# Kernel optimization log

Hardware: AMD Instinct MI355X
Metric: run time of the kernel (lower is better)

## Reference

```python
import jax, jax.numpy as jnp
import numpy as np

C = 1024      # channels
K = 7         # kernel_size
G = 1         # groups (G>1 crashes in the original torch code; see notes)
GC = C // G   # group_channels
OFFSET_SCALE = 2.0
LN_EPS = 1e-5


def setup_inputs() -> dict:
    key = jax.random.key(0)
    ks = jax.random.split(key, 8)
    N, L = 4, 2048
    s = 1.0 / np.sqrt(C)
    x = jax.random.normal(ks[0], (N, L, C), jnp.float32)
    Wi = jax.random.normal(ks[1], (C, C), jnp.float32) * s
    bi = jnp.zeros((C,), jnp.float32)
    dw_w = jax.random.normal(ks[2], (C, 1, 3), jnp.float32) * 0.5   # depthwise conv kernel (O, I/g=1, W)
    dw_b = jnp.zeros((C,), jnp.float32)
    ln_g = jnp.ones((C,), jnp.float32)
    ln_b = jnp.zeros((C,), jnp.float32)
    Wo = jax.random.normal(ks[3], (G * K, C), jnp.float32) * 0.02   # offset head (nonzero to exercise gather)
    bo = jnp.zeros((G * K,), jnp.float32)
    Wm = jax.random.normal(ks[4], (G * K, C), jnp.float32) * 0.02   # mask head
    bm = jnp.zeros((G * K,), jnp.float32)
    Wout = jax.random.normal(ks[5], (C, C), jnp.float32) * s
    bout = jnp.zeros((C,), jnp.float32)
    return {"x": x, "Wi": Wi, "bi": bi, "dw_w": dw_w, "dw_b": dw_b,
            "ln_g": ln_g, "ln_b": ln_b, "Wo": Wo, "bo": bo,
            "Wm": Wm, "bm": bm, "Wout": Wout, "bout": bout}


def _forward(x, Wi, bi, dw_w, dw_b, ln_g, ln_b, Wo, bo, Wm, bm, Wout, bout):
    N, L, Cc = x.shape
    dt = x.dtype
    # input projection
    x_proj = x @ Wi.T + bi                                  # [N,L,C]
    # depthwise conv (k=3, pad=1, groups=C) -> LayerNorm(C) -> GELU(exact)
    y = jax.lax.conv_general_dilated(
        x.transpose(0, 2, 1), dw_w, window_strides=(1,), padding=((1, 1),),
        dimension_numbers=("NCH", "OIH", "NCH"), feature_group_count=Cc)
    x_dw = y.transpose(0, 2, 1) + dw_b                       # [N,L,C]
    mu = x_dw.mean(-1, keepdims=True)
    var = ((x_dw - mu) ** 2).mean(-1, keepdims=True)
    x_dw = (x_dw - mu) * jax.lax.rsqrt(var + LN_EPS) * ln_g + ln_b
    x_dw = jax.nn.gelu(x_dw, approximate=False)
    # dynamic offsets and sampling mask
    offsets = (x_dw @ Wo.T + bo).reshape(N, L, G, K) * OFFSET_SCALE
    mask = jax.nn.softmax((x_dw @ Wm.T + bm).reshape(N, L, G, K), axis=-1)
    mask = jnp.nan_to_num(mask, nan=0.0)
    # absolute sampling positions
    ref_off = jnp.linspace(-(K // 2), K // 2, K).astype(dt)          # [K]
    pos = jnp.arange(L, dtype=dt)[None, :, None, None]               # [1,L,1,1]
    abs_pos = pos + ref_off[None, None, None, :] + offsets           # [N,L,G,K]
    apc = jnp.clip(abs_pos, 0.0, L - 1)
    p_floor = jnp.clip(apc.astype(jnp.int32), 0, L - 1)
    p_ceil = jnp.clip(p_floor + 1, 0, L - 1)
    w_ceil = apc - p_floor.astype(dt)
    w_floor = 1.0 - w_ceil
    valid = jnp.logical_not((abs_pos < 0) | (abs_pos > L - 1)).astype(dt)
    w_floor = w_floor * valid
    w_ceil = w_ceil * valid
    # gather + bilinear blend (G=1: each sample index grabs the full C channels)
    idx_f = p_floor.reshape(N, -1)[:, :, None]                       # [N, L*G*K, 1]
    idx_c = p_ceil.reshape(N, -1)[:, :, None]
    v_floor = jnp.take_along_axis(x_proj, idx_f, axis=1).reshape(N, L, G, K, GC)
    v_ceil = jnp.take_along_axis(x_proj, idx_c, axis=1).reshape(N, L, G, K, GC)
    sampled = v_floor * w_floor[..., None] + v_ceil * w_ceil[..., None]
    out = (sampled * mask[..., None]).sum(axis=3).reshape(N, L, Cc)  # sum over K
    return out @ Wout.T + bout


def reference(x, Wi, bi, dw_w, dw_b, ln_g, ln_b, Wo, bo, Wm, bm, Wout, bout):
    return _forward(x, Wi, bi, dw_w, dw_b, ln_g, ln_b, Wo, bo, Wm, bm, Wout, bout)
```

## Files before the change

### kernel.cpp

```cpp
#include <hip/hip_runtime.h>
#include <hip/hip_bf16.h>
#include <cstdint>

#define C_DIM 1024
#define L_DIM 2048
#define N_DIM 4
#define M_DIM (N_DIM * L_DIM)

typedef __attribute__((ext_vector_type(8))) short frag8;
typedef __attribute__((ext_vector_type(4)))  float f32x4;
typedef __attribute__((ext_vector_type(16))) float f32x16;

__device__ __forceinline__ void gl_lds16(const void* g, void* l) {
  __builtin_amdgcn_global_load_lds((const __attribute__((address_space(1))) void*)g,
                                   (__attribute__((address_space(3))) void*)l,
                                   16, 0, 0);
}
__device__ __forceinline__ void store_out(float* Y, size_t idx, float v) { Y[idx] = v; }
__device__ __forceinline__ void store_out(__hip_bfloat16* Y, size_t idx, float v) {
  Y[idx] = __float2bfloat16(v);
}
__device__ __forceinline__ float4 ldbf4(const __hip_bfloat16* p) {
  union { short4 s; __hip_bfloat16 h[4]; } u; u.s = *(const short4*)p;
  return make_float4((float)u.h[0], (float)u.h[1], (float)u.h[2], (float)u.h[3]);
}
__device__ __forceinline__ void stbf4(__hip_bfloat16* p, float4 v) {
  union { short4 s; __hip_bfloat16 h[4]; } u;
  u.h[0] = __float2bfloat16(v.x); u.h[1] = __float2bfloat16(v.y);
  u.h[2] = __float2bfloat16(v.z); u.h[3] = __float2bfloat16(v.w);
  *(short4*)p = u.s;
}
__device__ __forceinline__ float gelu_fast(float t) {
  const float t3 = t * t * t;
  const float ns = -1.5957691216f * t - 0.0713548163f * t3;
  return t / (1.f + __expf(ns));
}

__global__ __launch_bounds__(256)
void cvt_f32_bf16(const float* __restrict__ in, __hip_bfloat16* __restrict__ out, int n8) {
  const int i = blockIdx.x * 256 + threadIdx.x;
  if (i >= n8) return;
  const float4 a = *(const float4*)(in + (size_t)i * 8);
  const float4 b = *(const float4*)(in + (size_t)i * 8 + 4);
  union { __hip_bfloat16 h[8]; int4 q; } u;
  u.h[0] = __float2bfloat16(a.x); u.h[1] = __float2bfloat16(a.y);
  u.h[2] = __float2bfloat16(a.z); u.h[3] = __float2bfloat16(a.w);
  u.h[4] = __float2bfloat16(b.x); u.h[5] = __float2bfloat16(b.y);
  u.h[6] = __float2bfloat16(b.z); u.h[7] = __float2bfloat16(b.w);
  *(int4*)(out + (size_t)i * 8) = u.q;
}

__global__ __launch_bounds__(256)
void cvt_two_f32_bf16(const float* __restrict__ inA, __hip_bfloat16* __restrict__ outA,
                      const float* __restrict__ inB, __hip_bfloat16* __restrict__ outB,
                      int n8each) {
  int i = blockIdx.x * 256 + threadIdx.x;
  const float* in; __hip_bfloat16* out;
  if (i < n8each) { in = inA; out = outA; }
  else            { in = inB; out = outB; i -= n8each; }
  if (i >= n8each) return;
  const float4 a = *(const float4*)(in + (size_t)i * 8);
  const float4 b = *(const float4*)(in + (size_t)i * 8 + 4);
  union { __hip_bfloat16 h[8]; int4 q; } u;
  u.h[0] = __float2bfloat16(a.x); u.h[1] = __float2bfloat16(a.y);
  u.h[2] = __float2bfloat16(a.z); u.h[3] = __float2bfloat16(a.w);
  u.h[4] = __float2bfloat16(b.x); u.h[5] = __float2bfloat16(b.y);
  u.h[6] = __float2bfloat16(b.z); u.h[7] = __float2bfloat16(b.w);
  *(int4*)(out + (size_t)i * 8) = u.q;
}

__global__ __launch_bounds__(256)
void cvt_trans_wi(const float* __restrict__ Wi, __hip_bfloat16* __restrict__ WiT) {
  __shared__ float tile[64][65];
  const int bi = blockIdx.x;
  const int bj = blockIdx.y;
  const int t  = threadIdx.x;
  const int r  = t >> 2;
  const int c0 = (t & 3) * 16;
  const float* src = Wi + (size_t)(bi * 64 + r) * C_DIM + bj * 64 + c0;
  *(float4*)&tile[r][c0]      = *(const float4*)(src);
  *(float4*)&tile[r][c0 + 4]  = *(const float4*)(src + 4);
  *(float4*)&tile[r][c0 + 8]  = *(const float4*)(src + 8);
  *(float4*)&tile[r][c0 + 12] = *(const float4*)(src + 12);
  __syncthreads();
  const int kr = t >> 2, j0 = (t & 3) * 16;
  __hip_bfloat16* dst = WiT + (size_t)(bj * 64 + kr) * C_DIM + bi * 64 + j0;
  union { __hip_bfloat16 h[16]; int4 q[2]; } u;
#pragma unroll
  for (int i = 0; i < 16; i++) u.h[i] = __float2bfloat16(tile[j0 + i][kr]);
  *(int4*)(dst)     = u.q[0];
  *(int4*)(dst + 8) = u.q[1];
}

__global__ __launch_bounds__(256)
void cvt_wout_bvec(const float* __restrict__ Wout, __hip_bfloat16* __restrict__ Woutb,
                   const float* __restrict__ bi, float* __restrict__ bvec) {
  const int b = blockIdx.x;
  if (b < 512) {
    const int i = b * 256 + threadIdx.x;
    const float4 a = *(const float4*)(Wout + (size_t)i * 8);
    const float4 c = *(const float4*)(Wout + (size_t)i * 8 + 4);
    union { __hip_bfloat16 h[8]; int4 q; } u;
    u.h[0] = __float2bfloat16(a.x); u.h[1] = __float2bfloat16(a.y);
    u.h[2] = __float2bfloat16(a.z); u.h[3] = __float2bfloat16(a.w);
    u.h[4] = __float2bfloat16(c.x); u.h[5] = __float2bfloat16(c.y);
    u.h[6] = __float2bfloat16(c.z); u.h[7] = __float2bfloat16(c.w);
    *(int4*)(Woutb + (size_t)i * 8) = u.q;
  } else {
    const int row  = (b - 512) * 4 + (threadIdx.x >> 6);
    const int lane = threadIdx.x & 63;
    const float* wr = Wout + (size_t)row * C_DIM;
    float s = 0.f;
#pragma unroll
    for (int c = 0; c < 4; c++) {
      const int j = c * 256 + lane * 4;
      const float4 w  = *(const float4*)(wr + j);
      const float4 bb = *(const float4*)(bi + j);
      s += w.x * bb.x + w.y * bb.y + w.z * bb.z + w.w * bb.w;
    }
#pragma unroll
    for (int m = 1; m < 64; m <<= 1) s += __shfl_xor(s, m);
    if (lane == 0) bvec[row] = s;
  }
}

template <typename TY>
__global__ __launch_bounds__(256, 2)
void gemm_db(const __hip_bfloat16* __restrict__ X,
             const __hip_bfloat16* __restrict__ W,
             const float* __restrict__ bias,
             TY* __restrict__ Y, int M, int N, int K,
             const float* __restrict__ sArr, const float* __restrict__ bvec)
{
  __shared__ __hip_bfloat16 As[2][2][128 * 32];
  __shared__ __hip_bfloat16 Bs[2][2][128 * 32];
  const int tid  = threadIdx.x;
  const int lane = tid & 63;
  const int wave = tid >> 6;
  const int bm = blockIdx.x * 128;
  const int bn = blockIdx.y * 128;
  const int wr = (wave >> 1) * 64;
  const int wc = (wave & 1) * 64;
  const int srow  = tid >> 2;
  const int skoff = (tid & 3) * 8;

  const __hip_bfloat16* gA0 = X + (size_t)(bm + srow) * K + skoff;
  const __hip_bfloat16* gA1 = X + (size_t)(bm + 64 + srow) * K + skoff;
  const __hip_bfloat16* gB0 = W + (size_t)(bn + srow) * K + skoff;
  const __hip_bfloat16* gB1 = W + (size_t)(bn + 64 + srow) * K + skoff;

  f32x16 acc[2][2] = {};
  const int arow  = lane & 31;
  const int akoff = (lane >> 5) * 8;

#define STAGE(k0, buf)                                        \
  do {                                                        \
    gl_lds16(gA0 + (k0),      &As[buf][0][tid * 8]);          \
    gl_lds16(gA1 + (k0),      &As[buf][0][2048 + tid * 8]);   \
    gl_lds16(gA0 + (k0) + 32, &As[buf][1][tid * 8]);          \
    gl_lds16(gA1 + (k0) + 32, &As[buf][1][2048 + tid * 8]);   \
    gl_lds16(gB0 + (k0),      &Bs[buf][0][tid * 8]);          \
    gl_lds16(gB1 + (k0),      &Bs[buf][0][2048 + tid * 8]);   \
    gl_lds16(gB0 + (k0) + 32, &Bs[buf][1][tid * 8]);          \
    gl_lds16(gB1 + (k0) + 32, &Bs[buf][1][2048 + tid * 8]);   \
  } while (0)

  STAGE(0, 0);
  __syncthreads();
  const int iters = K / 64;
  for (int it = 0; it < iters; ++it) {
    const int cur = it & 1;
    if (it + 1 < iters) STAGE((it + 1) * 64, cur ^ 1);

#pragma unroll
    for (int p = 0; p < 2; ++p)
#pragma unroll
      for (int h = 0; h < 2; ++h) {
        const frag8 a0 = *(const frag8*)&As[cur][p][(wr + arow) * 32 + h * 16 + akoff];
        const frag8 a1 = *(const frag8*)&As[cur][p][(wr + 32 + arow) * 32 + h * 16 + akoff];
        const frag8 b0 = *(const frag8*)&Bs[cur][p][(wc + arow) * 32 + h * 16 + akoff];
        const frag8 b1 = *(const frag8*)&Bs[cur][p][(wc + 32 + arow) * 32 + h * 16 + akoff];
        acc[0][0] = __builtin_amdgcn_mfma_f32_32x32x16_bf16(a0, b0, acc[0][0], 0, 0, 0);
        acc[0][1] = __builtin_amdgcn_mfma_f32_32x32x16_bf16(a0, b1, acc[0][1], 0, 0, 0);
        acc[1][0] = __builtin_amdgcn_mfma_f32_32x32x16_bf16(a1, b0, acc[1][0], 0, 0, 0);
        acc[1][1] = __builtin_amdgcn_mfma_f32_32x32x16_bf16(a1, b1, acc[1][1], 0, 0, 0);
      }
    __syncthreads();
  }
#undef STAGE

#pragma unroll
  for (int i = 0; i < 2; i++)
#pragma unroll
    for (int j = 0; j < 2; j++) {
      const int col = bn + wc + j * 32 + (lane & 31);
      const float bv  = bias ? bias[col] : 0.f;
      const float bvv = (sArr && bvec) ? bvec[col] : 0.f;
#pragma unroll
      for (int r = 0; r < 16; r++) {
        const int row = bm + wr + i * 32 + (r & 3) + 8 * (r >> 2) + 4 * (lane >> 5);
        float extra = bv;
        if (sArr) extra += sArr[row] * bvv;
        store_out(Y, (size_t)row * N + col, acc[i][j][r] + extra);
      }
    }
}

struct Ld8f { float4 a, b; };
struct Ld8b { int4 a; };
__device__ __forceinline__ Ld8f ld8(const float* p) {
  return { *(const float4*)p, *(const float4*)(p + 4) };
}
__device__ __forceinline__ Ld8b ld8(const __hip_bfloat16* p) { return { *(const int4*)p }; }
__device__ __forceinline__ void st8(__hip_bfloat16* l, const Ld8f& v) {
  union { __hip_bfloat16 h[8]; int4 q; } u;
  u.h[0] = __float2bfloat16(v.a.x); u.h[1] = __float2bfloat16(v.a.y);
  u.h[2] = __float2bfloat16(v.a.z); u.h[3] = __float2bfloat16(v.a.w);
  u.h[4] = __float2bfloat16(v.b.x); u.h[5] = __float2bfloat16(v.b.y);
  u.h[6] = __float2bfloat16(v.b.z); u.h[7] = __float2bfloat16(v.b.w);
  *(int4*)l = u.q;
}
__device__ __forceinline__ void st8(__hip_bfloat16* l, const Ld8b& v) { *(int4*)l = v.a; }

template <typename TX, typename TY>
__global__ __launch_bounds__(256, 2)
void gemm_nt(const TX* __restrict__ X, const float* __restrict__ W,
             const float* __restrict__ bias, TY* __restrict__ Y, int M, int N, int K)
{
  __shared__ __hip_bfloat16 As[128 * 32];
  __shared__ __hip_bfloat16 Bs[128 * 32];
  const int tid  = threadIdx.x;
  const int lane = tid & 63;
  const int wave = tid >> 6;
  const int bm = blockIdx.x * 128;
  const int bn = blockIdx.y * 128;
  const int wr = (wave >> 1) * 64;
  const int wc = (wave & 1) * 64;
  const int srow  = tid >> 2;
  const int skoff = (tid & 3) * 8;

  f32x4 acc[4][4] = {};
  const TX*    gA0 = X + (size_t)(bm + srow) * K + skoff;
  const TX*    gA1 = X + (size_t)(bm + 64 + srow) * K + skoff;
  const float* gB0 = W + (size_t)(bn + srow) * K + skoff;
  const float* gB1 = W + (size_t)(bn + 64 + srow) * K + skoff;
  const int arow  = lane & 15;
  const int akoff = (lane >> 4) * 8;

  for (int k0 = 0; k0 < K; k0 += 32) {
    const auto va0 = ld8(gA0 + k0);
    const auto va1 = ld8(gA1 + k0);
    const auto vb0 = ld8(gB0 + k0);
    const auto vb1 = ld8(gB1 + k0);
    __syncthreads();
    st8(&As[srow * 32 + skoff],        va0);
    st8(&As[(64 + srow) * 32 + skoff], va1);
    st8(&Bs[srow * 32 + skoff],        vb0);
    st8(&Bs[(64 + srow) * 32 + skoff], vb1);
    __syncthreads();

    frag8 a[4], b[4];
#pragma unroll
    for (int i = 0; i < 4; i++)
      a[i] = *(const frag8*)&As[(wr + i * 16 + arow) * 32 + akoff];
#pragma unroll
    for (int j = 0; j < 4; j++)
      b[j] = *(const frag8*)&Bs[(wc + j * 16 + arow) * 32 + akoff];
#pragma unroll
    for (int i = 0; i < 4; i++)
#pragma unroll
      for (int j = 0; j < 4; j++)
        acc[i][j] = __builtin_amdgcn_mfma_f32_16x16x32_bf16(a[i], b[j], acc[i][j], 0, 0, 0);
  }
#pragma unroll
  for (int i = 0; i < 4; i++)
#pragma unroll
    for (int j = 0; j < 4; j++) {
      const int col = bn + wc + j * 16 + (lane & 15);
      const float bv = bias[col];
#pragma unroll
      for (int r = 0; r < 4; r++) {
        const int row = bm + wr + i * 16 + (lane >> 4) * 4 + r;
        store_out(Y, (size_t)row * N + col, acc[i][j][r] + bv);
      }
    }
}

__global__ __launch_bounds__(512, 2)
void pre_fused_v4(const float* __restrict__ x,
                  const float* __restrict__ dw_w, const float* __restrict__ dw_b,
                  const float* __restrict__ ln_g, const float* __restrict__ ln_b,
                  const float* __restrict__ Wo,   const float* __restrict__ bo,
                  const float* __restrict__ Wm,   const float* __restrict__ bmb,
                  __hip_bfloat16* __restrict__ xbb,
                  float* __restrict__ coef)
{
  __shared__ float sW[16384];
  float* sWo  = sW;
  float* sWm  = sW + 7168;
  float* slng = sW + 14336;
  float* slnb = sW + 15360;

  const int tid  = threadIdx.x;
  const int lane = tid & 63;
  const int wid  = tid >> 6;

#pragma unroll
  for (int i = 0; i < 3; i++) {
    gl_lds16(Wo + (size_t)(i * 512 + tid) * 4, &sWo[(i * 512 + tid) * 4]);
    gl_lds16(Wm + (size_t)(i * 512 + tid) * 4, &sWm[(i * 512 + tid) * 4]);
  }
  if (tid < 256) {
    gl_lds16(Wo + (size_t)(1536 + tid) * 4, &sWo[(1536 + tid) * 4]);
    gl_lds16(Wm + (size_t)(1536 + tid) * 4, &sWm[(1536 + tid) * 4]);
    gl_lds16(ln_g + (size_t)tid * 4, &slng[tid * 4]);
  } else {
    const int t = tid - 256;
    gl_lds16(ln_b + (size_t)t * 4, &slnb[t * 4]);
  }
  __syncthreads();

  const int b    = blockIdx.x;
  const int bs   = (b & 7) * 64 + (b >> 3);
  const int row0 = bs * 16 + wid * 2;
  const int l0   = row0 & (L_DIM - 1);

  const float* xr = x + (size_t)row0 * C_DIM;

  float4 v[2][4];
#pragma unroll
  for (int j = 0; j < 4; j++) {
    const int c4 = j * 256 + lane * 4;
    float4 xv[4];
#pragma unroll
    for (int m = 0; m < 4; m++) {
      const int lm = l0 + m - 1;
      if (lm >= 0 && lm < L_DIM)
        xv[m] = *(const float4*)(xr + ((long)m - 1) * C_DIM + c4);
      else
        xv[m] = make_float4(0.f, 0.f, 0.f, 0.f);
    }
#pragma unroll
    for (int r = 0; r < 2; r++)
      stbf4(xbb + (size_t)(row0 + r) * C_DIM + c4, xv[r + 1]);

    const float4 w0 = *(const float4*)(dw_w + (size_t)c4 * 3);
    const float4 w1 = *(const float4*)(dw_w + (size_t)c4 * 3 + 4);
    const float4 w2 = *(const float4*)(dw_w + (size_t)c4 * 3 + 8);
    const float4 bb = *(const float4*)(dw_b + c4);
#pragma unroll
    for (int r = 0; r < 2; r++) {
      const float4 xm = xv[r], x0 = xv[r + 1], xq = xv[r + 2];
      v[r][j].x = xm.x * w0.x + x0.x * w0.y + xq.x * w0.z + bb.x;
      v[r][j].y = xm.y * w0.w + x0.y * w1.x + xq.y * w1.y + bb.y;
      v[r][j].z = xm.z * w1.z + x0.z * w1.w + xq.z * w2.x + bb.z;
      v[r][j].w = xm.w * w2.y + x0.w * w2.z + xq.w * w2.w + bb.w;
    }
  }

  float mu[2], rstd[2];
#pragma unroll
  for (int r = 0; r < 2; r++) {
    float s1 = 0.f, s2 = 0.f;
#pragma unroll
    for (int j = 0; j < 4; j++) {
      s1 += v[r][j].x + v[r][j].y + v[r][j].z + v[r][j].w;
      s2 += v[r][j].x * v[r][j].x + v[r][j].y * v[r][j].y
          + v[r][j].z * v[r][j].z + v[r][j].w * v[r][j].w;
    }
    const float t1 = s1 + __shfl_xor(s1, 32);
    const float t2 = s2 + __shfl_xor(s2, 32);
    float cc = (lane < 32) ? t1 : t2;
#pragma unroll
    for (int m = 16; m >= 1; m >>= 1) cc += __shfl_xor(cc, m);
    const float dd = __shfl_xor(cc, 32);
    const float S1 = (lane < 32) ? cc : dd;
    const float S2 = (lane < 32) ? dd : cc;
    mu[r]   = S1 * (1.f / C_DIM);
    rstd[r] = rsqrtf(S2 * (1.f / C_DIM) - mu[r] * mu[r] + 1e-5f);
  }

  float po[2][7] = {}, pm[2][7] = {};
#pragma unroll
  for (int j = 0; j < 4; j++) {
    const int c4 = j * 256 + lane * 4;
    const float4 gg = *(const float4*)&slng[c4];
    const float4 bb = *(const float4*)&slnb[c4];
    float4 g[2];
#pragma unroll
    for (int r = 0; r < 2; r++) {
      g[r].x = gelu_fast((v[r][j].x - mu[r]) * rstd[r] * gg.x + bb.x);
      g[r].y = gelu_fast((v[r][j].y - mu[r]) * rstd[r] * gg.y + bb.y);
      g[r].z = gelu_fast((v[r][j].z - mu[r]) * rstd[r] * gg.z + bb.z);
      g[r].w = gelu_fast((v[r][j].w - mu[r]) * rstd[r] * gg.w + bb.w);
    }
#pragma unroll
    for (int k = 0; k < 7; k++) {
      const float4 wo = *(const float4*)&sWo[k * 1024 + c4];
      const float4 wm = *(const float4*)&sWm[k * 1024 + c4];
#pragma unroll
      for (int r = 0; r < 2; r++) {
        po[r][k] += g[r].x * wo.x + g[r].y * wo.y + g[r].z * wo.z + g[r].w * wo.w;
        pm[r][k] += g[r].x * wm.x + g[r].y * wm.y + g[r].z * wm.z + g[r].w * wm.w;
      }
    }
  }

  float poS[2][7], pmS[2][7];
#pragma unroll
  for (int r = 0; r < 2; r++)
#pragma unroll
    for (int k = 0; k < 7; k++) {
      const float tp = po[r][k] + __shfl_xor(po[r][k], 32);
      const float tm = pm[r][k] + __shfl_xor(pm[r][k], 32);
      float cc = (lane < 32) ? tp : tm;
#pragma unroll
      for (int m = 16; m >= 1; m >>= 1) cc += __shfl_xor(cc, m);
      const float dd = __shfl_xor(cc, 32);
      poS[r][k] = (lane < 32) ? cc : dd;
      pmS[r][k] = (lane < 32) ? dd : cc;
    }

#pragma unroll
  for (int r = 0; r < 2; r++) {
    float lg[7], mx = -1e30f;
#pragma unroll
    for (int k = 0; k < 7; k++) { lg[k] = pmS[r][k] + bmb[k]; mx = fmaxf(mx, lg[k]); }
    float se = 0.f, e[7];
#pragma unroll
    for (int k = 0; k < 7; k++) { e[k] = __expf(lg[k] - mx); se += e[k]; }
    const float inv = 1.f / se;
    const int l = l0 + r;

    if (lane == r) {
      float pk[32];
#pragma unroll
      for (int k = 0; k < 7; k++) {
        const float msk = e[k] * inv;
        const float off = (poS[r][k] + bo[k]) * 2.0f;
        const float ap  = (float)l + (float)(k - 3) + off;
        const float apc = fminf(fmaxf(ap, 0.f), (float)(L_DIM - 1));
        int f = (int)apc;
        int c = f + 1; if (c > L_DIM - 1) c = L_DIM - 1;
        const float w1  = apc - (float)f;
        const float val = (ap < 0.f || ap > (float)(L_DIM - 1)) ? 0.f : 1.f;
        pk[k]      = (1.f - w1) * val * msk;
        pk[8 + k]  = w1 * val * msk;
        pk[16 + k] = (float)f;
        pk[24 + k] = (float)c;
      }
      pk[7] = pk[15] = pk[23] = pk[31] = 0.f;
      float* cr = coef + (size_t)(row0 + r) * 32;
#pragma unroll
      for (int q = 0; q < 8; q++)
        *(float4*)(cr + q * 4) = make_float4(pk[q*4], pk[q*4+1], pk[q*4+2], pk[q*4+3]);
    }
  }
}

__global__ __launch_bounds__(256)
void gather_g(const float* __restrict__ coef,
              const __hip_bfloat16* __restrict__ xbb,
              __hip_bfloat16* __restrict__ gb,
              float* __restrict__ sArr)
{
  const int b    = blockIdx.x;
  const int bs   = (b & 7) * 256 + (b >> 3);
  const int wid  = threadIdx.x >> 6;
  const int lane = threadIdx.x & 63;
  const int row  = bs * 4 + wid;
  const int n    = row >> 11;

  const float* cr = coef + (size_t)row * 32;
  const float4 q0 = *(const float4*)(cr);
  const float4 q1 = *(const float4*)(cr + 4);
  const float4 q2 = *(const float4*)(cr + 8);
  const float4 q3 = *(const float4*)(cr + 12);
  const float4 q4 = *(const float4*)(cr + 16);
  const float4 q5 = *(const float4*)(cr + 20);
  const float4 q6 = *(const float4*)(cr + 24);
  const float4 q7 = *(const float4*)(cr + 28);

  const float wf[7] = {q0.x, q0.y, q0.z, q0.w, q1.x, q1.y, q1.z};
  const float wc[7] = {q2.x, q2.y, q2.z, q2.w, q3.x, q3.y, q3.z};
  const int   pf[7] = {(int)q4.x, (int)q4.y, (int)q4.z, (int)q4.w, (int)q5.x, (int)q5.y, (int)q5.z};
  const int   pc[7] = {(int)q6.x, (int)q6.y, (int)q6.z, (int)q6.w, (int)q7.x, (int)q7.y, (int)q7.z};

  if (lane == 0) {
    sArr[row] = q0.x + q0.y + q0.z + q0.w + q1.x + q1.y + q1.z
              + q2.x + q2.y + q2.z + q2.w + q3.x + q3.y + q3.z;
  }

  const __hip_bfloat16* xpn = xbb + ((size_t)n * L_DIM) * C_DIM;
  __hip_bfloat16* so = gb + (size_t)row * C_DIM;

#pragma unroll
  for (int j = 0; j < 2; j++) {
    const int c8 = j * 512 + lane * 8;
    float a[8] = {0.f, 0.f, 0.f, 0.f, 0.f, 0.f, 0.f, 0.f};
#pragma unroll
    for (int k = 0; k < 7; k++) {
      union { int4 q; __hip_bfloat16 h[8]; } uf, uc;
      uf.q = *(const int4*)(xpn + (size_t)pf[k] * C_DIM + c8);
      uc.q = *(const int4*)(xpn + (size_t)pc[k] * C_DIM + c8);
#pragma unroll
      for (int t = 0; t < 8; t++)
        a[t] += wf[k] * (float)uf.h[t] + wc[k] * (float)uc.h[t];
    }
    union { int4 q; __hip_bfloat16 h[8]; } uo;
#pragma unroll
    for (int t = 0; t < 8; t++) uo.h[t] = __float2bfloat16(a[t]);
    *(int4*)(so + c8) = uo.q;
  }
}

__global__ __launch_bounds__(256)
void mid_fused_v4(const float* __restrict__ x,
                  const float* __restrict__ dw_w, const float* __restrict__ dw_b,
                  const float* __restrict__ ln_g, const float* __restrict__ ln_b,
                  const float* __restrict__ Wo,   const float* __restrict__ bo,
                  const float* __restrict__ Wm,   const float* __restrict__ bmb,
                  const __hip_bfloat16* __restrict__ xp,
                  __hip_bfloat16* __restrict__ smp)
{
  const int b    = blockIdx.x;
  const int bs   = (b & 7) * 256 + (b >> 3);
  const int wid  = threadIdx.x >> 6;
  const int lane = threadIdx.x & 63;
  const int row  = bs * 4 + wid;
  const int l    = row & (L_DIM - 1);
  const int n    = row >> 11;

  const float* xr = x + (size_t)row * C_DIM;

  float4 v[4];
#pragma unroll
  for (int j = 0; j < 4; j++) {
    const int c4 = j * 256 + lane * 4;
    const float4 x0 = *(const float4*)(xr + c4);
    float4 xm = make_float4(0.f, 0.f, 0.f, 0.f);
    float4 xq = make_float4(0.f, 0.f, 0.f, 0.f);
    if (l > 0)         xm = *(const float4*)(xr + c4 - C_DIM);
    if (l < L_DIM - 1) xq = *(const float4*)(xr + c4 + C_DIM);
    const float4 w0 = *(const float4*)(dw_w + (size_t)c4 * 3);
    const float4 w1 = *(const float4*)(dw_w + (size_t)c4 * 3 + 4);
    const float4 w2 = *(const float4*)(dw_w + (size_t)c4 * 3 + 8);
    const float4 bb = *(const float4*)(dw_b + c4);
    v[j].x = xm.x * w0.x + x0.x * w0.y + xq.x * w0.z + bb.x;
    v[j].y = xm.y * w0.w + x0.y * w1.x + xq.y * w1.y + bb.y;
    v[j].z = xm.z * w1.z + x0.z * w1.w + xq.z * w2.x + bb.z;
    v[j].w = xm.w * w2.y + x0.w * w2.z + xq.w * w2.w + bb.w;
  }

  float s1 = 0.f, s2 = 0.f;
#pragma unroll
  for (int j = 0; j < 4; j++) {
    s1 += v[j].x + v[j].y + v[j].z + v[j].w;
    s2 += v[j].x * v[j].x + v[j].y * v[j].y + v[j].z * v[j].z + v[j].w * v[j].w;
  }
#pragma unroll
  for (int m = 1; m < 64; m <<= 1) { s1 += __shfl_xor(s1, m); s2 += __shfl_xor(s2, m); }
  const float mu   = s1 * (1.f / C_DIM);
  const float rstd = rsqrtf(s2 * (1.f / C_DIM) - mu * mu + 1e-5f);

  float4 g[4];
#pragma unroll
  for (int j = 0; j < 4; j++) {
    const int c4 = j * 256 + lane * 4;
    const float4 gg = *(const float4*)(ln_g + c4);
    const float4 bb = *(const float4*)(ln_b + c4);
    g[j].x = gelu_fast((v[j].x - mu) * rstd * gg.x + bb.x);
    g[j].y = gelu_fast((v[j].y - mu) * rstd * gg.y + bb.y);
    g[j].z = gelu_fast((v[j].z - mu) * rstd * gg.z + bb.z);
    g[j].w = gelu_fast((v[j].w - mu) * rstd * gg.w + bb.w);
  }

  float po[7] = {0,0,0,0,0,0,0}, pm[7] = {0,0,0,0,0,0,0};
#pragma unroll
  for (int k = 0; k < 7; k++) {
#pragma unroll
    for (int j = 0; j < 4; j++) {
      const int c4 = j * 256 + lane * 4;
      const float4 wo = *(const float4*)(Wo + (size_t)k * C_DIM + c4);
      const float4 wm = *(const float4*)(Wm + (size_t)k * C_DIM + c4);
      po[k] += g[j].x * wo.x + g[j].y * wo.y + g[j].z * wo.z + g[j].w * wo.w;
      pm[k] += g[j].x * wm.x + g[j].y * wm.y + g[j].z * wm.z + g[j].w * wm.w;
    }
  }
#pragma unroll
  for (int k = 0; k < 7; k++)
#pragma unroll
    for (int m = 1; m < 64; m <<= 1) {
      po[k] += __shfl_xor(po[k], m);
      pm[k] += __shfl_xor(pm[k], m);
    }

  float lg[7], mx = -1e30f;
#pragma unroll
  for (int k = 0; k < 7; k++) { lg[k] = pm[k] + bmb[k]; mx = fmaxf(mx, lg[k]); }
  float se = 0.f, e[7];
#pragma unroll
  for (int k = 0; k < 7; k++) { e[k] = __expf(lg[k] - mx); se += e[k]; }
  const float inv = 1.f / se;

  float wf[7], wcl[7]; int pf[7], pc[7];
#pragma unroll
  for (int k = 0; k < 7; k++) {
    const float msk = e[k] * inv;
    const float off = (po[k] + bo[k]) * 2.0f;
    const float ap  = (float)l + (float)(k - 3) + off;
    const float apc = fminf(fmaxf(ap, 0.f), (float)(L_DIM - 1));
    int f = (int)apc;
    int c = f + 1; if (c > L_DIM - 1) c = L_DIM - 1;
    const float w1  = apc - (float)f;
    const float val = (ap < 0.f || ap > (float)(L_DIM - 1)) ? 0.f : 1.f;
    wf[k]  = (1.f - w1) * val * msk;
    wcl[k] = w1 * val * msk;
    pf[k] = f; pc[k] = c;
  }

  const __hip_bfloat16* xpn = xp + ((size_t)n * L_DIM) * C_DIM;
  __hip_bfloat16* so = smp + (size_t)row * C_DIM;
#pragma unroll
  for (int j = 0; j < 4; j++) {
    const int c4 = j * 256 + lane * 4;
    float4 a = make_float4(0.f, 0.f, 0.f, 0.f);
#pragma unroll
    for (int k = 0; k < 7; k++) {
      const float4 vf = ldbf4(xpn + (size_t)pf[k] * C_DIM + c4);
      const float4 vc = ldbf4(xpn + (size_t)pc[k] * C_DIM + c4);
      a.x += wf[k] * vf.x + wcl[k] * vc.x;
      a.y += wf[k] * vf.y + wcl[k] * vc.y;
      a.z += wf[k] * vf.z + wcl[k] * vc.z;
      a.w += wf[k] * vf.w + wcl[k] * vc.w;
    }
    stbf4(so + c4, a);
  }
}

extern "C" void kernel_launch(void* const* d_in, const int* in_sizes, int n_in,
                              void* d_out, int out_size, void* d_ws, size_t ws_size,
                              hipStream_t stream)
{
  const float* x    = (const float*)d_in[0];
  const float* Wi   = (const float*)d_in[1];
  const float* bi   = (const float*)d_in[2];
  const float* dw_w = (const float*)d_in[3];
  const float* dw_b = (const float*)d_in[4];
  const float* ln_g = (const float*)d_in[5];
  const float* ln_b = (const float*)d_in[6];
  const float* Wo   = (const float*)d_in[7];
  const float* bo   = (const float*)d_in[8];
  const float* Wm   = (const float*)d_in[9];
  const float* bm   = (const float*)d_in[10];
  const float* Wout = (const float*)d_in[11];
  const float* bout = (const float*)d_in[12];
  float* out = (float*)d_out;

  const size_t XE = (size_t)M_DIM * C_DIM;
  const size_t WE = (size_t)C_DIM * C_DIM;
  char* wsb = (char*)d_ws;

  __hip_bfloat16* xbb2  = (__hip_bfloat16*)wsb;
  __hip_bfloat16* gb    = (__hip_bfloat16*)(wsb + XE * 2);
  __hip_bfloat16* Woutb2= (__hip_bfloat16*)(wsb + XE * 4);
  __hip_bfloat16* WiT   = (__hip_bfloat16*)(wsb + XE * 4 + WE * 2);
  __hip_bfloat16* Wcb   = (__hip_bfloat16*)(wsb + XE * 4 + WE * 4);
  float* coef2 = (float*)(wsb + XE * 4 + WE * 6);
  float* sArr  = (float*)(wsb + XE * 4 + WE * 6 + (size_t)M_DIM * 128);
  float* bvec  = (float*)(wsb + XE * 4 + WE * 6 + (size_t)M_DIM * 128 + (size_t)M_DIM * 4);
  const size_t need_v5 = XE * 4 + WE * 6 + (size_t)M_DIM * 132 + 4096;

  __hip_bfloat16* xp    = (__hip_bfloat16*)wsb;
  __hip_bfloat16* smp   = (__hip_bfloat16*)(wsb + XE * 2);
  __hip_bfloat16* Wib   = (__hip_bfloat16*)(wsb + XE * 4);
  __hip_bfloat16* Woutb = (__hip_bfloat16*)(wsb + XE * 4 + WE * 2);
  __hip_bfloat16* xbb   = (__hip_bfloat16*)(wsb + XE * 4 + WE * 4);
  const size_t need_w2   = XE * 4 + WE * 4;
  const size_t need_full = need_w2 + XE * 2;

  dim3 gg(M_DIM / 128, C_DIM / 128);

  if (ws_size >= need_v5) {
    cvt_trans_wi<<<dim3(16, 16), 256, 0, stream>>>(Wi, WiT);
    cvt_wout_bvec<<<768, 256, 0, stream>>>(Wout, Woutb2, bi, bvec);
    gemm_db<__hip_bfloat16><<<dim3(8, 8), 256, 0, stream>>>(
        Woutb2, WiT, nullptr, Wcb, C_DIM, C_DIM, C_DIM, nullptr, nullptr);
    pre_fused_v4<<<M_DIM / 16, 512, 0, stream>>>(
        x, dw_w, dw_b, ln_g, ln_b, Wo, bo, Wm, bm, xbb2, coef2);
    gather_g<<<M_DIM / 4, 256, 0, stream>>>(coef2, xbb2, gb, sArr);
    gemm_db<float><<<gg, 256, 0, stream>>>(
        gb, Wcb, bout, out, M_DIM, C_DIM, C_DIM, sArr, bvec);
  } else if (ws_size >= need_full) {
    cvt_f32_bf16<<<(int)(XE / 8 / 256), 256, 0, stream>>>(x, xbb, (int)(XE / 8));
    cvt_two_f32_bf16<<<(int)(2 * (WE / 8) / 256), 256, 0, stream>>>(
        Wi, Wib, Wout, Woutb, (int)(WE / 8));
    gemm_db<__hip_bfloat16><<<gg, 256, 0, stream>>>(xbb, Wib, bi, xp, M_DIM, C_DIM, C_DIM,
                                                    nullptr, nullptr);
    mid_fused_v4<<<M_DIM / 4, 256, 0, stream>>>(x, dw_w, dw_b, ln_g, ln_b, Wo, bo, Wm, bm, xp, smp);
    gemm_db<float><<<gg, 256, 0, stream>>>(smp, Woutb, bout, out, M_DIM, C_DIM, C_DIM,
                                           nullptr, nullptr);
  } else if (ws_size >= need_w2) {
    cvt_f32_bf16<<<(int)(WE / 8 / 256), 256, 0, stream>>>(Wout, Woutb, (int)(WE / 8));
    gemm_nt<float, __hip_bfloat16><<<gg, 256, 0, stream>>>(x, Wi, bi, xp, M_DIM, C_DIM, C_DIM);
    mid_fused_v4<<<M_DIM / 4, 256, 0, stream>>>(x, dw_w, dw_b, ln_g, ln_b, Wo, bo, Wm, bm, xp, smp);
    gemm_db<float><<<gg, 256, 0, stream>>>(smp, Woutb, bout, out, M_DIM, C_DIM, C_DIM,
                                           nullptr, nullptr);
  } else {
    gemm_nt<float, __hip_bfloat16><<<gg, 256, 0, stream>>>(x, Wi, bi, xp, M_DIM, C_DIM, C_DIM);
    mid_fused_v4<<<M_DIM / 4, 256, 0, stream>>>(x, dw_w, dw_b, ln_g, ln_b, Wo, bo, Wm, bm, xp, smp);
    gemm_nt<__hip_bfloat16, float><<<gg, 256, 0, stream>>>(smp, Wout, bout, out, M_DIM, C_DIM, C_DIM);
  }
}
```

Measured before the change: 201.9 us.

## Merge weight prep into pre-kernel and weight-combine GEMM into gather kernel

Folds the Wi transpose/convert, Wout convert and bias-vector kernels into the pre-processing kernel as extra block ranges, and runs the Wout·Wi weight-combine GEMM as the first 64 blocks of the gather kernel using 32x32 MFMA. This cuts five launches down to two and lets the small weight work overlap with the activation work instead of running serially. In exchange, the GEMM blocks idle half their waves (the extra waves spin on matching barriers), and the gather blocks change from 4 to 8 rows per block.

```diff
diff --git a/kernel.cpp b/kernel.cpp
--- a/kernel.cpp
+++ b/kernel.cpp
@@ -67,61 +67,6 @@
   u.h[4] = __float2bfloat16(b.x); u.h[5] = __float2bfloat16(b.y);
   u.h[6] = __float2bfloat16(b.z); u.h[7] = __float2bfloat16(b.w);
   *(int4*)(out + (size_t)i * 8) = u.q;
-}
-
-__global__ __launch_bounds__(256)
-void cvt_trans_wi(const float* __restrict__ Wi, __hip_bfloat16* __restrict__ WiT) {
-  __shared__ float tile[64][65];
-  const int bi = blockIdx.x;
-  const int bj = blockIdx.y;
-  const int t  = threadIdx.x;
-  const int r  = t >> 2;
-  const int c0 = (t & 3) * 16;
-  const float* src = Wi + (size_t)(bi * 64 + r) * C_DIM + bj * 64 + c0;
-  *(float4*)&tile[r][c0]      = *(const float4*)(src);
-  *(float4*)&tile[r][c0 + 4]  = *(const float4*)(src + 4);
-  *(float4*)&tile[r][c0 + 8]  = *(const float4*)(src + 8);
-  *(float4*)&tile[r][c0 + 12] = *(const float4*)(src + 12);
-  __syncthreads();
-  const int kr = t >> 2, j0 = (t & 3) * 16;
-  __hip_bfloat16* dst = WiT + (size_t)(bj * 64 + kr) * C_DIM + bi * 64 + j0;
-  union { __hip_bfloat16 h[16]; int4 q[2]; } u;
-#pragma unroll
-  for (int i = 0; i < 16; i++) u.h[i] = __float2bfloat16(tile[j0 + i][kr]);
-  *(int4*)(dst)     = u.q[0];
-  *(int4*)(dst + 8) = u.q[1];
-}
-
-__global__ __launch_bounds__(256)
-void cvt_wout_bvec(const float* __restrict__ Wout, __hip_bfloat16* __restrict__ Woutb,
-                   const float* __restrict__ bi, float* __restrict__ bvec) {
-  const int b = blockIdx.x;
-  if (b < 512) {
-    const int i = b * 256 + threadIdx.x;
-    const float4 a = *(const float4*)(Wout + (size_t)i * 8);
-    const float4 c = *(const float4*)(Wout + (size_t)i * 8 + 4);
-    union { __hip_bfloat16 h[8]; int4 q; } u;
-    u.h[0] = __float2bfloat16(a.x); u.h[1] = __float2bfloat16(a.y);
-    u.h[2] = __float2bfloat16(a.z); u.h[3] = __float2bfloat16(a.w);
-    u.h[4] = __float2bfloat16(c.x); u.h[5] = __float2bfloat16(c.y);
-    u.h[6] = __float2bfloat16(c.z); u.h[7] = __float2bfloat16(c.w);
-    *(int4*)(Woutb + (size_t)i * 8) = u.q;
-  } else {
-    const int row  = (b - 512) * 4 + (threadIdx.x >> 6);
-    const int lane = threadIdx.x & 63;
-    const float* wr = Wout + (size_t)row * C_DIM;
-    float s = 0.f;
-#pragma unroll
-    for (int c = 0; c < 4; c++) {
-      const int j = c * 256 + lane * 4;
-      const float4 w  = *(const float4*)(wr + j);
-      const float4 bb = *(const float4*)(bi + j);
-      s += w.x * bb.x + w.y * bb.y + w.z * bb.z + w.w * bb.w;
-    }
-#pragma unroll
-    for (int m = 1; m < 64; m <<= 1) s += __shfl_xor(s, m);
-    if (lane == 0) bvec[row] = s;
-  }
 }
 
 template <typename TY>
@@ -287,23 +232,79 @@
 }
 
 __global__ __launch_bounds__(512, 2)
-void pre_fused_v4(const float* __restrict__ x,
-                  const float* __restrict__ dw_w, const float* __restrict__ dw_b,
-                  const float* __restrict__ ln_g, const float* __restrict__ ln_b,
-                  const float* __restrict__ Wo,   const float* __restrict__ bo,
-                  const float* __restrict__ Wm,   const float* __restrict__ bmb,
-                  __hip_bfloat16* __restrict__ xbb,
-                  float* __restrict__ coef)
+void fused_pre_prep(const float* __restrict__ x,
+                    const float* __restrict__ dw_w, const float* __restrict__ dw_b,
+                    const float* __restrict__ ln_g, const float* __restrict__ ln_b,
+                    const float* __restrict__ Wo,   const float* __restrict__ bo,
+                    const float* __restrict__ Wm,   const float* __restrict__ bmb,
+                    const float* __restrict__ Wi,   const float* __restrict__ Wout,
+                    const float* __restrict__ bi,
+                    __hip_bfloat16* __restrict__ xbb,
+                    float* __restrict__ coef,
+                    __hip_bfloat16* __restrict__ WiT,
+                    __hip_bfloat16* __restrict__ Woutb,
+                    float* __restrict__ bvec)
 {
-  __shared__ float sW[16384];
-  float* sWo  = sW;
-  float* sWm  = sW + 7168;
-  float* slng = sW + 14336;
-  float* slnb = sW + 15360;
-
+  __shared__ float smem[16384];
+  const int blk  = blockIdx.x;
   const int tid  = threadIdx.x;
   const int lane = tid & 63;
   const int wid  = tid >> 6;
+
+  if (blk >= 1024) {
+    const int vb = blk - 1024;
+#pragma unroll
+    for (int rr = 0; rr < 8; rr++) {
+      const int row = vb * 64 + wid * 8 + rr;
+      const float* wr_ = Wout + (size_t)row * C_DIM;
+      float s = 0.f;
+#pragma unroll
+      for (int c = 0; c < 4; c++) {
+        const int j = c * 256 + lane * 4;
+        const float4 w  = *(const float4*)(wr_ + j);
+        const float4 bb = *(const float4*)(bi + j);
+        s += w.x * bb.x + w.y * bb.y + w.z * bb.z + w.w * bb.w;
+      }
+#pragma unroll
+      for (int m = 1; m < 64; m <<= 1) s += __shfl_xor(s, m);
+      if (lane == 0) bvec[row] = s;
+    }
+    return;
+  }
+  if (blk >= 768) {
+    const int idx = (blk - 768) * 512 + tid;
+    const float4 a = *(const float4*)(Wout + (size_t)idx * 8);
+    const float4 c = *(const float4*)(Wout + (size_t)idx * 8 + 4);
+    union { __hip_bfloat16 h[8]; int4 q; } u;
+    u.h[0] = __float2bfloat16(a.x); u.h[1] = __float2bfloat16(a.y);
+    u.h[2] = __float2bfloat16(a.z); u.h[3] = __float2bfloat16(a.w);
+    u.h[4] = __float2bfloat16(c.x); u.h[5] = __float2bfloat16(c.y);
+    u.h[6] = __float2bfloat16(c.z); u.h[7] = __float2bfloat16(c.w);
+    *(int4*)(Woutb + (size_t)idx * 8) = u.q;
+    return;
+  }
+  if (blk >= 512) {
+    float (*tile)[65] = (float(*)[65])smem;
+    const int tb  = blk - 512;
+    const int bi_ = tb >> 4;
+    const int bj  = tb & 15;
+    const int r   = tid >> 3;
+    const int c0  = (tid & 7) * 8;
+    const float* src = Wi + (size_t)(bi_ * 64 + r) * C_DIM + bj * 64 + c0;
+    *(float4*)&tile[r][c0]     = *(const float4*)(src);
+    *(float4*)&tile[r][c0 + 4] = *(const float4*)(src + 4);
+    __syncthreads();
+    union { __hip_bfloat16 h[8]; int4 q; } u;
+#pragma unroll
+    for (int i = 0; i < 8; i++) u.h[i] = __float2bfloat16(tile[c0 + i][r]);
+    *(int4*)(WiT + (size_t)(bj * 64 + r) * C_DIM + bi_ * 64 + c0) = u.q;
+    return;
+  }
+
+  float* sWo  = smem;
+  float* sWm  = smem + 7168;
+  float* slng = smem + 14336;
+  float* slnb = smem + 15360;
 
 #pragma unroll
   for (int i = 0; i < 3; i++) {
@@ -320,11 +321,9 @@
   }
   __syncthreads();
 
-  const int b    = blockIdx.x;
-  const int bs   = (b & 7) * 64 + (b >> 3);
+  const int bs   = (blk & 7) * 64 + (blk >> 3);
   const int row0 = bs * 16 + wid * 2;
   const int l0   = row0 & (L_DIM - 1);
-
   const float* xr = x + (size_t)row0 * C_DIM;
 
   float4 v[2][4];
@@ -458,18 +457,95 @@
   }
 }
 
-__global__ __launch_bounds__(256)
-void gather_g(const float* __restrict__ coef,
-              const __hip_bfloat16* __restrict__ xbb,
-              __hip_bfloat16* __restrict__ gb,
-              float* __restrict__ sArr)
+__global__ __launch_bounds__(512, 2)
+void wcomb_gather(const __hip_bfloat16* __restrict__ Woutb,
+                  const __hip_bfloat16* __restrict__ WiT,
+                  __hip_bfloat16* __restrict__ Wcb,
+                  const float* __restrict__ coef,
+                  const __hip_bfloat16* __restrict__ xbb,
+                  __hip_bfloat16* __restrict__ gb,
+                  float* __restrict__ sArr)
 {
-  const int b    = blockIdx.x;
-  const int bs   = (b & 7) * 256 + (b >> 3);
-  const int wid  = threadIdx.x >> 6;
-  const int lane = threadIdx.x & 63;
-  const int row  = bs * 4 + wid;
-  const int n    = row >> 11;
+  __shared__ __hip_bfloat16 As[2][2][128 * 32];
+  __shared__ __hip_bfloat16 Bs[2][2][128 * 32];
+  const int tid  = threadIdx.x;
+  const int lane = tid & 63;
+  const int wid  = tid >> 6;
+
+  if (blockIdx.x < 64) {
+    if (wid >= 4) {
+      for (int i = 0; i < 17; i++) __syncthreads();
+      return;
+    }
+    const int bm = (int)(blockIdx.x >> 3) * 128;
+    const int bn = (int)(blockIdx.x & 7) * 128;
+    const int wr = (wid >> 1) * 64;
+    const int wc = (wid & 1) * 64;
+    const int srow  = tid >> 2;
+    const int skoff = (tid & 3) * 8;
+    const int K = C_DIM;
+
+    const __hip_bfloat16* gA0 = Woutb + (size_t)(bm + srow) * K + skoff;
+    const __hip_bfloat16* gA1 = Woutb + (size_t)(bm + 64 + srow) * K + skoff;
+    const __hip_bfloat16* gB0 = WiT   + (size_t)(bn + srow) * K + skoff;
+    const __hip_bfloat16* gB1 = WiT   + (size_t)(bn + 64 + srow) * K + skoff;
+
+    f32x16 acc[2][2] = {};
+    const int arow  = lane & 31;
+    const int akoff = (lane >> 5) * 8;
+
+#define WSTAGE(k0, buf)                                       \
+  do {                                                        \
+    gl_lds16(gA0 + (k0),      &As[buf][0][tid * 8]);          \
+    gl_lds16(gA1 + (k0),      &As[buf][0][2048 + tid * 8]);   \
+    gl_lds16(gA0 + (k0) + 32, &As[buf][1][tid * 8]);          \
+    gl_lds16(gA1 + (k0) + 32, &As[buf][1][2048 + tid * 8]);   \
+    gl_lds16(gB0 + (k0),      &Bs[buf][0][tid * 8]);          \
+    gl_lds16(gB1 + (k0),      &Bs[buf][0][2048 + tid * 8]);   \
+    gl_lds16(gB0 + (k0) + 32, &Bs[buf][1][tid * 8]);          \
+    gl_lds16(gB1 + (k0) + 32, &Bs[buf][1][2048 + tid * 8]);   \
+  } while (0)
+
+    WSTAGE(0, 0);
+    __syncthreads();
+    for (int it = 0; it < 16; ++it) {
+      const int cur = it & 1;
+      if (it + 1 < 16) WSTAGE((it + 1) * 64, cur ^ 1);
+#pragma unroll
+      for (int p = 0; p < 2; ++p)
+#pragma unroll
+        for (int h = 0; h < 2; ++h) {
+          const frag8 a0 = *(const frag8*)&As[cur][p][(wr + arow) * 32 + h * 16 + akoff];
+          const frag8 a1 = *(const frag8*)&As[cur][p][(wr + 32 + arow) * 32 + h * 16 + akoff];
+          const frag8 b0 = *(const frag8*)&Bs[cur][p][(wc + arow) * 32 + h * 16 + akoff];
+          const frag8 b1 = *(const frag8*)&Bs[cur][p][(wc + 32 + arow) * 32 + h * 16 + akoff];
+          acc[0][0] = __builtin_amdgcn_mfma_f32_32x32x16_bf16(a0, b0, acc[0][0], 0, 0, 0);
+          acc[0][1] = __builtin_amdgcn_mfma_f32_32x32x16_bf16(a0, b1, acc[0][1], 0, 0, 0);
+          acc[1][0] = __builtin_amdgcn_mfma_f32_32x32x16_bf16(a1, b0, acc[1][0], 0, 0, 0);
+          acc[1][1] = __builtin_amdgcn_mfma_f32_32x32x16_bf16(a1, b1, acc[1][1], 0, 0, 0);
+        }
+      __syncthreads();
+    }
+#undef WSTAGE
+
+#pragma unroll
+    for (int i = 0; i < 2; i++)
+#pragma unroll
+      for (int j = 0; j < 2; j++) {
+        const int col = bn + wc + j * 32 + (lane & 31);
+#pragma unroll
+        for (int r = 0; r < 16; r++) {
+          const int row = bm + wr + i * 32 + (r & 3) + 8 * (r >> 2) + 4 * (lane >> 5);
+          Wcb[(size_t)row * C_DIM + col] = __float2bfloat16(acc[i][j][r]);
+        }
+      }
+    return;
+  }
+
+  const int b   = (int)blockIdx.x - 64;
+  const int bs  = (b & 7) * 128 + (b >> 3);
+  const int row = bs * 8 + wid;
+  const int n   = row >> 11;
 
   const float* cr = coef + (size_t)row * 32;
   const float4 q0 = *(const float4*)(cr);
@@ -682,13 +758,11 @@
   dim3 gg(M_DIM / 128, C_DIM / 128);
 
   if (ws_size >= need_v5) {
-    cvt_trans_wi<<<dim3(16, 16), 256, 0, stream>>>(Wi, WiT);
-    cvt_wout_bvec<<<768, 256, 0, stream>>>(Wout, Woutb2, bi, bvec);
-    gemm_db<__hip_bfloat16><<<dim3(8, 8), 256, 0, stream>>>(
-        Woutb2, WiT, nullptr, Wcb, C_DIM, C_DIM, C_DIM, nullptr, nullptr);
-    pre_fused_v4<<<M_DIM / 16, 512, 0, stream>>>(
-        x, dw_w, dw_b, ln_g, ln_b, Wo, bo, Wm, bm, xbb2, coef2);
-    gather_g<<<M_DIM / 4, 256, 0, stream>>>(coef2, xbb2, gb, sArr);
+    fused_pre_prep<<<1040, 512, 0, stream>>>(
+        x, dw_w, dw_b, ln_g, ln_b, Wo, bo, Wm, bm,
+        Wi, Wout, bi, xbb2, coef2, WiT, Woutb2, bvec);
+    wcomb_gather<<<1088, 512, 0, stream>>>(
+        Woutb2, WiT, Wcb, coef2, xbb2, gb, sArr);
     gemm_db<float><<<gg, 256, 0, stream>>>(
         gb, Wcb, bout, out, M_DIM, C_DIM, C_DIM, sArr, bvec);
   } else if (ws_size >= need_full) {
```

Result: faster. 185.3 us (-8.2%).
